# Kernel tuning notes

Measured on AMD Instinct MI355X. Metric: run time of the kernel, lower is better.

## Reference

```python
import jax, jax.numpy as jnp
import numpy as np

E = 256   # embed_dim
H = 8     # num_heads
D = E // H  # head_dim = 32
L = 1024  # seq len (Q_len == K_len == V_len)


def setup_inputs() -> dict:
    key = jax.random.key(0)
    ks = jax.random.split(key, 10)
    f = lambda k, s: jax.random.normal(k, s, dtype=jnp.float32)
    return {
        "V": f(ks[0], (L, E)),
        "K": f(ks[1], (L, E)),
        "Q": f(ks[2], (L, E)),
        # genomic-style coordinates, strictly positive
        "position": jax.random.uniform(ks[3], (L,), dtype=jnp.float32) * 1e5,
        "Wq": f(ks[4], (E, E)) * 0.02,
        "Wk": f(ks[5], (E, E)) * 0.02,
        "Wv": f(ks[6], (E, E)) * 0.02,
        "Wr": f(ks[7], (E, 1)) * 0.02,   # K_relative_linear weight [out=E, in=1]
        "Wo": f(ks[8], (E, E)) * 0.02,
        "bo": jnp.zeros((E,), jnp.float32),
    }


def reference(V, K, Q, position, Wq, Wk, Wv, Wr, Wo, bo):
    Lq = Q.shape[0]
    # projections (nn.Linear: x @ W.T), split into heads -> (L, H, D)
    q = (Q @ Wq.T).reshape(Lq, H, D)
    k = (K @ Wk.T).reshape(Lq, H, D)
    v = (V @ Wv.T).reshape(Lq, H, D)

    # relative position scalar per (q, k) pair: log(|p_q - p_k| + 1)
    rel = jnp.log(jnp.abs(position[:, None] - position[None, :]) + 1.0)  # (L, L)

    # K_relative_linear maps scalar rel -> (H, D); the einsum
    # 'nqhd,nhqjd->nhqj' then factorizes exactly as:
    #   sum_d Q[q,h,d] * rel[q,j] * Wr[h,d] = (Q . Wr)[h,q] * rel[q,j]
    # so we avoid materializing the (H, L, L, D) tensor while computing
    # mathematically identical results.
    Wr_h = Wr[:, 0].reshape(H, D)                    # (H, D)
    coeff = jnp.einsum('qhd,hd->hq', q, Wr_h)        # (H, L)

    energy = jnp.einsum('qhd,khd->hqk', q, k)        # (H, L, L)
    energy = energy + coeff[:, :, None] * rel[None, :, :]

    attn = jax.nn.softmax(energy / np.float32(E) ** 0.5, axis=2)
    out = jnp.einsum('hqk,khd->qhd', attn, v).reshape(Lq, E)
    out = out @ Wo.T + bo
    return out
```

## Files before the change

kernel.cpp:

```cpp
#include <hip/hip_runtime.h>
#include <math.h>

#define EDIM 256
#define LDIM 1024
#define HDIM 8
#define DDIM 32

typedef __attribute__((ext_vector_type(8))) short short8;
typedef __attribute__((ext_vector_type(4))) short shortx4;
typedef __attribute__((ext_vector_type(4))) float f32x4;

__device__ inline unsigned short bf16h(float x) {
    unsigned u = __float_as_uint(x);
    return (unsigned short)((u + 0x7fff + ((u >> 16) & 1)) >> 16);
}
__device__ inline float bf16tof(unsigned short h) {
    return __uint_as_float(((unsigned)h) << 16);
}
__device__ inline float exp2fast(float x) {
    float r; asm volatile("v_exp_f32 %0, %1" : "=v"(r) : "v"(x)); return r;
}
__device__ inline float log2fast(float x) {
    float r; asm volatile("v_log_f32 %0, %1" : "=v"(r) : "v"(x)); return r;
}

#define SC2 0.09016843880556021f

__global__ __launch_bounds__(256) void proj_kernel(
    const float* __restrict__ Q, const float* __restrict__ Km, const float* __restrict__ V,
    const float* __restrict__ Wq, const float* __restrict__ Wk, const float* __restrict__ Wv,
    const float* __restrict__ Wr, const float* __restrict__ Wo,
    short* __restrict__ qThi, short* __restrict__ qTlo,
    short* __restrict__ kThi, short* __restrict__ kTlo,
    short* __restrict__ vThi, short* __restrict__ vTlo,
    float* __restrict__ coeff, short* __restrict__ Wohi, short* __restrict__ Wolo)
{
    const int z = blockIdx.z;
    const int tid = threadIdx.x;

    if (z == 3) {
        const int idx = ((blockIdx.y * 32 + blockIdx.x) << 8) + tid;
        const float w = Wo[idx];
        const unsigned short hh = bf16h(w);
        Wohi[idx] = (short)hh;
        Wolo[idx] = (short)bf16h(w - bf16tof(hh));
        return;
    }

    const float* __restrict__ X = (z == 0) ? Q : (z == 1) ? Km : V;
    const float* __restrict__ W = (z == 0) ? Wq : (z == 1) ? Wk : Wv;
    short* __restrict__ dhi     = (z == 0) ? qThi : (z == 1) ? kThi : vThi;
    short* __restrict__ dlo     = (z == 0) ? qTlo : (z == 1) ? kTlo : vTlo;

    const int n0 = blockIdx.x * 32;
    const int o0 = blockIdx.y * 32;
    const int wave = tid >> 6, lane = tid & 63;
    const int n = lane & 15, quad = lane >> 4;
    const int rh = wave & 1, oh = wave >> 1;

    const int s    = tid >> 7;
    const int r    = (tid >> 2) & 31;
    const int qd   = tid & 3;
    const int half = r >> 4;
    const int fl8  = ((r & 15) | (qd << 4)) * 8;

    __shared__ short Xhi[2][2][512], Xlo[2][2][512];
    __shared__ short Whi[2][2][512], Wlo[2][2][512];
    __shared__ float cpart[2][2][16];

    const float* xp = X + (n0 + r) * EDIM + s * 32 + qd * 8;
    const float* wp = W + (o0 + r) * EDIM + s * 32 + qd * 8;

    float4 xa0 = *(const float4*)xp, xa1 = *(const float4*)(xp + 4);
    float4 wa0 = *(const float4*)wp, wa1 = *(const float4*)(wp + 4);

    f32x4 acc = {0.f, 0.f, 0.f, 0.f};

    for (int kb = 0; kb < EDIM; kb += 64) {
        __syncthreads();
        {
            float xv[8] = {xa0.x,xa0.y,xa0.z,xa0.w, xa1.x,xa1.y,xa1.z,xa1.w};
            float wv[8] = {wa0.x,wa0.y,wa0.z,wa0.w, wa1.x,wa1.y,wa1.z,wa1.w};
            short8 xh, xl, wh, wl;
            #pragma unroll
            for (int j = 0; j < 8; ++j) {
                unsigned short xhh = bf16h(xv[j]);
                unsigned short whh = bf16h(wv[j]);
                xh[j] = (short)xhh; xl[j] = (short)bf16h(xv[j] - bf16tof(xhh));
                wh[j] = (short)whh; wl[j] = (short)bf16h(wv[j] - bf16tof(whh));
            }
            *(short8*)&Xhi[s][half][fl8] = xh;
            *(short8*)&Xlo[s][half][fl8] = xl;
            *(short8*)&Whi[s][half][fl8] = wh;
            *(short8*)&Wlo[s][half][fl8] = wl;
        }
        float4 xn0, xn1, wn0, wn1;
        if (kb + 64 < EDIM) {
            xn0 = *(const float4*)(xp + kb + 64); xn1 = *(const float4*)(xp + kb + 68);
            wn0 = *(const float4*)(wp + kb + 64); wn1 = *(const float4*)(wp + kb + 68);
        }
        __syncthreads();
        #pragma unroll
        for (int ss = 0; ss < 2; ++ss) {
            short8 ah = *(const short8*)&Xhi[ss][rh][lane*8];
            short8 al = *(const short8*)&Xlo[ss][rh][lane*8];
            short8 bh = *(const short8*)&Whi[ss][oh][lane*8];
            short8 bl = *(const short8*)&Wlo[ss][oh][lane*8];
            acc = __builtin_amdgcn_mfma_f32_16x16x32_bf16(al, bh, acc, 0, 0, 0);
            acc = __builtin_amdgcn_mfma_f32_16x16x32_bf16(ah, bl, acc, 0, 0, 0);
            acc = __builtin_amdgcn_mfma_f32_16x16x32_bf16(ah, bh, acc, 0, 0, 0);
        }
        xa0 = xn0; xa1 = xn1; wa0 = wn0; wa1 = wn1;
    }

    const int h  = o0 >> 5;
    const int og = oh * 16 + n;
    #pragma unroll
    for (int i = 0; i < 4; ++i) {
        const int row = rh * 16 + 4 * quad + i;
        const unsigned short hh = bf16h(acc[i]);
        dhi[(h * LDIM + n0 + row) * DDIM + og] = (short)hh;
        dlo[(h * LDIM + n0 + row) * DDIM + og] = (short)bf16h(acc[i] - bf16tof(hh));
    }

    if (z == 0) {
        const float wr = Wr[o0 + og];
        #pragma unroll
        for (int i = 0; i < 4; ++i) {
            float c = acc[i] * wr;
            c += __shfl_xor(c, 1, 64);
            c += __shfl_xor(c, 2, 64);
            c += __shfl_xor(c, 4, 64);
            c += __shfl_xor(c, 8, 64);
            if (n == 0) cpart[rh][oh][4*quad + i] = c;
        }
        __syncthreads();
        if (tid < 32)
            coeff[h * LDIM + n0 + tid] = cpart[tid >> 4][0][tid & 15]
                                       + cpart[tid >> 4][1][tid & 15];
    }
}

__global__ __launch_bounds__(256, 4) void attn_kernel(
    const short* __restrict__ qThi, const short* __restrict__ qTlo,
    const short* __restrict__ kThi, const short* __restrict__ kTlo,
    const short* __restrict__ vThi, const short* __restrict__ vTlo,
    const float* __restrict__ coeff, const float* __restrict__ pos,
    float* __restrict__ Op, float* __restrict__ Mp, float* __restrict__ Lp, int nkt)
{
    const int h   = blockIdx.y;
    const int q0  = blockIdx.x * 64;
    const int p   = blockIdx.z;
    const int kt0 = p * nkt * 64;
    const int tid  = threadIdx.x;
    const int wave = tid >> 6;
    const int lane = tid & 63;
    const int n    = lane & 15;
    const int quad = lane >> 4;
    const int qs0  = wave * 16;

    __shared__ __align__(16) short khi[4*64*8];
    __shared__ __align__(16) short klo[4*64*8];
    __shared__ __align__(16) short vs_hi[32][72];
    __shared__ __align__(16) short vs_lo[32][72];
    __shared__ __align__(16) short pa_hi[64][72];
    __shared__ __align__(16) short pa_lo[64][72];
    __shared__ float pk[64];

    const short8 qhi = *(const short8*)(qThi + (h*LDIM + q0 + qs0 + n) * DDIM + quad*8);
    const short8 qlo = *(const short8*)(qTlo + (h*LDIM + q0 + qs0 + n) * DDIM + quad*8);

    float pq[4], cq[4];
    #pragma unroll
    for (int i = 0; i < 4; ++i) {
        const int r = q0 + qs0 + 4*quad + i;
        pq[i] = pos[r];
        cq[i] = coeff[h*LDIM + r] * 0.0625f;
    }

    float m[4], l[4];
    #pragma unroll
    for (int i = 0; i < 4; ++i) { m[i] = -INFINITY; l[i] = 0.f; }

    f32x4 of0 = {0.f,0.f,0.f,0.f}, of1 = {0.f,0.f,0.f,0.f};

    const int cS = tid >> 2;
    const int dq = tid & 3;
    const int lane2 = (cS & 15) | (dq << 4);
    const int gS = cS >> 4;

    short8 khi_c, klo_c, vhi_c, vlo_c; float pkc = 0.f;
    {
        const int off = (h*LDIM + kt0 + cS) * DDIM + dq*8;
        khi_c = *(const short8*)(kThi + off);
        klo_c = *(const short8*)(kTlo + off);
        vhi_c = *(const short8*)(vThi + off);
        vlo_c = *(const short8*)(vTlo + off);
        if (tid < 64) pkc = pos[kt0 + tid];
    }

    for (int t = 0; t < nkt; ++t) {
        __syncthreads();

        *((short8*)&khi[(gS*64 + lane2)*8]) = khi_c;
        *((short8*)&klo[(gS*64 + lane2)*8]) = klo_c;
        #pragma unroll
        for (int j = 0; j < 8; ++j) {
            vs_hi[dq*8 + j][cS] = vhi_c[j];
            vs_lo[dq*8 + j][cS] = vlo_c[j];
        }
        if (tid < 64) pk[tid] = pkc;

        short8 khi_n, klo_n, vhi_n, vlo_n; float pkn = 0.f;
        if (t + 1 < nkt) {
            const int off = (h*LDIM + kt0 + (t+1)*64 + cS) * DDIM + dq*8;
            khi_n = *(const short8*)(kThi + off);
            klo_n = *(const short8*)(kTlo + off);
            vhi_n = *(const short8*)(vThi + off);
            vlo_n = *(const short8*)(vTlo + off);
            if (tid < 64) pkn = pos[kt0 + (t+1)*64 + tid];
        }
        __syncthreads();

        f32x4 Sf[4];
        #pragma unroll
        for (int t4 = 0; t4 < 4; ++t4) {
            short8 bhi = *((const short8*)&khi[(t4*64 + lane)*8]);
            short8 blo = *((const short8*)&klo[(t4*64 + lane)*8]);
            f32x4 acc = {0.f, 0.f, 0.f, 0.f};
            acc = __builtin_amdgcn_mfma_f32_16x16x32_bf16(qlo, bhi, acc, 0, 0, 0);
            acc = __builtin_amdgcn_mfma_f32_16x16x32_bf16(qhi, blo, acc, 0, 0, 0);
            acc = __builtin_amdgcn_mfma_f32_16x16x32_bf16(qhi, bhi, acc, 0, 0, 0);
            Sf[t4] = acc;
        }

        float ev[4][4];
        float rmax[4] = {-INFINITY, -INFINITY, -INFINITY, -INFINITY};
        #pragma unroll
        for (int t4 = 0; t4 < 4; ++t4) {
            const float pkt = pk[16*t4 + n];
            #pragma unroll
            for (int i = 0; i < 4; ++i) {
                float s = fmaf(Sf[t4][i], SC2, cq[i] * log2fast(fabsf(pq[i] - pkt) + 1.f));
                ev[t4][i] = s;
                rmax[i] = fmaxf(rmax[i], s);
            }
        }
        #pragma unroll
        for (int off = 1; off < 16; off <<= 1)
            #pragma unroll
            for (int i = 0; i < 4; ++i)
                rmax[i] = fmaxf(rmax[i], __shfl_xor(rmax[i], off, 64));

        float al[4], rsum[4];
        #pragma unroll
        for (int i = 0; i < 4; ++i) {
            const float mn = fmaxf(m[i], rmax[i]);
            al[i] = exp2fast(m[i] - mn);
            m[i] = mn;
            rsum[i] = 0.f;
        }
        #pragma unroll
        for (int t4 = 0; t4 < 4; ++t4)
            #pragma unroll
            for (int i = 0; i < 4; ++i) {
                float e = exp2fast(ev[t4][i] - m[i]);
                rsum[i] += e;
                unsigned u = __float_as_uint(e);
                pa_hi[qs0 + 4*quad + i][16*t4 + n] = (short)(u >> 16);
                float r = e - __uint_as_float(u & 0xffff0000u);
                pa_lo[qs0 + 4*quad + i][16*t4 + n] = (short)bf16h(r);
            }
        #pragma unroll
        for (int off = 1; off < 16; off <<= 1)
            #pragma unroll
            for (int i = 0; i < 4; ++i)
                rsum[i] += __shfl_xor(rsum[i], off, 64);
        #pragma unroll
        for (int i = 0; i < 4; ++i) l[i] = l[i]*al[i] + rsum[i];

        #pragma unroll
        for (int i = 0; i < 4; ++i) { of0[i] *= al[i]; of1[i] *= al[i]; }

        #pragma unroll
        for (int ch = 0; ch < 2; ++ch) {
            short8 phi = *(const short8*)&pa_hi[qs0 + n][ch*32 + quad*8];
            short8 plo = *(const short8*)&pa_lo[qs0 + n][ch*32 + quad*8];
            #pragma unroll
            for (int dt = 0; dt < 2; ++dt) {
                short8 vh8 = *(const short8*)&vs_hi[dt*16 + n][ch*32 + quad*8];
                short8 vl8 = *(const short8*)&vs_lo[dt*16 + n][ch*32 + quad*8];
                f32x4& of = dt ? of1 : of0;
                of = __builtin_amdgcn_mfma_f32_16x16x32_bf16(plo, vh8, of, 0, 0, 0);
                of = __builtin_amdgcn_mfma_f32_16x16x32_bf16(phi, vl8, of, 0, 0, 0);
                of = __builtin_amdgcn_mfma_f32_16x16x32_bf16(phi, vh8, of, 0, 0, 0);
            }
        }

        khi_c = khi_n; klo_c = klo_n; vhi_c = vhi_n; vlo_c = vlo_n; pkc = pkn;
    }

    const int ph = p * HDIM + h;
    {
        const size_t base = ((size_t)ph * LDIM + q0 + qs0) * DDIM;
        #pragma unroll
        for (int i = 0; i < 4; ++i) {
            Op[base + (size_t)(4*quad + i)*DDIM + n]      = of0[i];
            Op[base + (size_t)(4*quad + i)*DDIM + 16 + n] = of1[i];
        }
    }
    if (n == 0) {
        #pragma unroll
        for (int i = 0; i < 4; ++i) {
            const int r = q0 + qs0 + 4*quad + i;
            Mp[ph*LDIM + r] = m[i];
            Lp[ph*LDIM + r] = l[i];
        }
    }
}

__global__ __launch_bounds__(256) void combine_kernel(
    const float* __restrict__ Op, const float* __restrict__ Mp, const float* __restrict__ Lp,
    int P, short* __restrict__ Ahi, short* __restrict__ Alo)
{
    const int idx = blockIdx.x * 256 + threadIdx.x;
    const int n  = idx >> 6;
    const int e4 = (idx & 63) * 4;
    const int h  = e4 >> 5;
    const int d  = e4 & 31;

    float mv[8], lv[8];
    float mx = -INFINITY;
    #pragma unroll
    for (int p = 0; p < 8; ++p) if (p < P) {
        mv[p] = Mp[(p*HDIM + h)*LDIM + n];
        lv[p] = Lp[(p*HDIM + h)*LDIM + n];
        mx = fmaxf(mx, mv[p]);
    }
    float s = 0.f;
    #pragma unroll
    for (int p = 0; p < 8; ++p) if (p < P) {
        float a = exp2fast(mv[p] - mx);
        mv[p] = a;
        s += a * lv[p];
    }
    const float inv = 1.f / s;

    float4 x; x.x = x.y = x.z = x.w = 0.f;
    #pragma unroll
    for (int p = 0; p < 8; ++p) if (p < P) {
        const float sp = mv[p] * inv;
        float4 xp = *(const float4*)(Op + ((size_t)(p*HDIM + h)*LDIM + n)*DDIM + d);
        x.x += sp*xp.x; x.y += sp*xp.y; x.z += sp*xp.z; x.w += sp*xp.w;
    }
    float a4[4] = {x.x, x.y, x.z, x.w};
    shortx4 ah4, al4;
    #pragma unroll
    for (int j = 0; j < 4; ++j) {
        const unsigned short hh = bf16h(a4[j]);
        ah4[j] = (short)hh;
        al4[j] = (short)bf16h(a4[j] - bf16tof(hh));
    }
    *(shortx4*)(Ahi + n*EDIM + e4) = ah4;
    *(shortx4*)(Alo + n*EDIM + e4) = al4;
}

__global__ __launch_bounds__(256) void outproj_kernel(
    const short* __restrict__ Ahi, const short* __restrict__ Alo,
    const short* __restrict__ Wohi, const short* __restrict__ Wolo,
    const float* __restrict__ bo, float* __restrict__ out)
{
    const int n0 = blockIdx.x * 32;
    const int o0 = blockIdx.y * 32;
    const int tid = threadIdx.x;
    const int wave = tid >> 6, lane = tid & 63;
    const int n = lane & 15, quad = lane >> 4;
    const int rh = wave & 1, oh = wave >> 1;

    const int s    = tid >> 7;
    const int r    = (tid >> 2) & 31;
    const int qd   = tid & 3;
    const int half = r >> 4;
    const int fl8  = ((r & 15) | (qd << 4)) * 8;

    __shared__ short Xhi[2][2][512], Xlo[2][2][512];
    __shared__ short Whi[2][2][512], Wlo[2][2][512];

    const short* xph = Ahi  + (n0 + r) * EDIM + s * 32 + qd * 8;
    const short* xpl = Alo  + (n0 + r) * EDIM + s * 32 + qd * 8;
    const short* wph = Wohi + (o0 + r) * EDIM + s * 32 + qd * 8;
    const short* wpl = Wolo + (o0 + r) * EDIM + s * 32 + qd * 8;

    short8 xh_c = *(const short8*)xph;
    short8 xl_c = *(const short8*)xpl;
    short8 wh_c = *(const short8*)wph;
    short8 wl_c = *(const short8*)wpl;

    f32x4 acc = {0.f, 0.f, 0.f, 0.f};

    for (int kb = 0; kb < EDIM; kb += 64) {
        __syncthreads();
        *(short8*)&Xhi[s][half][fl8] = xh_c;
        *(short8*)&Xlo[s][half][fl8] = xl_c;
        *(short8*)&Whi[s][half][fl8] = wh_c;
        *(short8*)&Wlo[s][half][fl8] = wl_c;
        short8 xh_n, xl_n, wh_n, wl_n;
        if (kb + 64 < EDIM) {
            xh_n = *(const short8*)(xph + kb + 64);
            xl_n = *(const short8*)(xpl + kb + 64);
            wh_n = *(const short8*)(wph + kb + 64);
            wl_n = *(const short8*)(wpl + kb + 64);
        }
        __syncthreads();
        #pragma unroll
        for (int ss = 0; ss < 2; ++ss) {
            short8 ah = *(const short8*)&Xhi[ss][rh][lane*8];
            short8 al = *(const short8*)&Xlo[ss][rh][lane*8];
            short8 bh = *(const short8*)&Whi[ss][oh][lane*8];
            short8 bl = *(const short8*)&Wlo[ss][oh][lane*8];
            acc = __builtin_amdgcn_mfma_f32_16x16x32_bf16(al, bh, acc, 0, 0, 0);
            acc = __builtin_amdgcn_mfma_f32_16x16x32_bf16(ah, bl, acc, 0, 0, 0);
            acc = __builtin_amdgcn_mfma_f32_16x16x32_bf16(ah, bh, acc, 0, 0, 0);
        }
        xh_c = xh_n; xl_c = xl_n; wh_c = wh_n; wl_c = wl_n;
    }

    const int og = o0 + oh*16 + n;
    const float b = bo[og];
    #pragma unroll
    for (int i = 0; i < 4; ++i) {
        const int row = n0 + rh*16 + 4*quad + i;
        out[row * EDIM + og] = acc[i] + b;
    }
}

extern "C" void kernel_launch(void* const* d_in, const int* in_sizes, int n_in,
                              void* d_out, int out_size, void* d_ws, size_t ws_size,
                              hipStream_t stream) {
    const float* V   = (const float*)d_in[0];
    const float* K   = (const float*)d_in[1];
    const float* Q   = (const float*)d_in[2];
    const float* pos = (const float*)d_in[3];
    const float* Wq  = (const float*)d_in[4];
    const float* Wk  = (const float*)d_in[5];
    const float* Wv  = (const float*)d_in[6];
    const float* Wr  = (const float*)d_in[7];
    const float* Wo  = (const float*)d_in[8];
    const float* bo  = (const float*)d_in[9];
    float* out = (float*)d_out;
    char* base = (char*)d_ws;

    auto need = [](int P) -> size_t { return 3440640 + (size_t)P * 1114112; };
    int P = 2;
    if (ws_size >= need(8)) P = 8;
    else if (ws_size >= need(4)) P = 4;

    short* qThi  = (short*)(base);
    short* qTlo  = (short*)(base + 524288);
    short* kThi  = (short*)(base + 1048576);
    short* kTlo  = (short*)(base + 1572864);
    short* vThi  = (short*)(base + 2097152);
    short* vTlo  = (short*)(base + 2621440);
    float* coeff = (float*)(base + 3145728);
    short* Wohi  = (short*)(base + 3178496);
    short* Wolo  = (short*)(base + 3309568);
    float* Op    = (float*)(base + 3440640);
    float* Mp    = Op + (size_t)P * 262144;
    float* Lp    = Mp + (size_t)P * 8192;
    short* Ahi   = qThi;
    short* Alo   = qTlo;

    proj_kernel   <<<dim3(32, 8, 4), 256, 0, stream>>>(Q, K, V, Wq, Wk, Wv, Wr, Wo,
                                                       qThi, qTlo, kThi, kTlo, vThi, vTlo,
                                                       coeff, Wohi, Wolo);
    attn_kernel   <<<dim3(16, 8, P), 256, 0, stream>>>(qThi, qTlo, kThi, kTlo, vThi, vTlo,
                                                       coeff, pos, Op, Mp, Lp, 16 / P);
    combine_kernel<<<dim3(256),      256, 0, stream>>>(Op, Mp, Lp, P, Ahi, Alo);
    outproj_kernel<<<dim3(32, 8),    256, 0, stream>>>(Ahi, Alo, Wohi, Wolo, bo, out);
}
```

Before: 104.6 us.

## Fuse split-K combine into attention with intra-block per-wave key splits

The attention kernel now gives each block 16 queries and splits the 1024 keys across its 4 waves, each wave running its own online softmax over 256 keys. The per-wave partial outputs, maxima and sums are merged in shared memory, and the result is written directly as bf16 hi/lo into A. This removes the separate combine kernel, one launch, and the global round-trip of partial outputs. In exchange K and the key positions are read straight from global memory with no shared staging, V is transposed per wave, and launch bounds drop to 2 blocks per CU.

```diff
diff --git a/kernel.cpp b/kernel.cpp
--- a/kernel.cpp
+++ b/kernel.cpp
@@ -7,6 +7,7 @@
 #define DDIM 32
 
 typedef __attribute__((ext_vector_type(8))) short short8;
+typedef __attribute__((ext_vector_type(2))) short short2v;
 typedef __attribute__((ext_vector_type(4))) short shortx4;
 typedef __attribute__((ext_vector_type(4))) float f32x4;
 
@@ -141,39 +142,35 @@
     }
 }
 
-__global__ __launch_bounds__(256, 4) void attn_kernel(
+__global__ __launch_bounds__(256, 2) void attn_kernel(
     const short* __restrict__ qThi, const short* __restrict__ qTlo,
     const short* __restrict__ kThi, const short* __restrict__ kTlo,
     const short* __restrict__ vThi, const short* __restrict__ vTlo,
     const float* __restrict__ coeff, const float* __restrict__ pos,
-    float* __restrict__ Op, float* __restrict__ Mp, float* __restrict__ Lp, int nkt)
+    short* __restrict__ Ahi, short* __restrict__ Alo)
 {
-    const int h   = blockIdx.y;
-    const int q0  = blockIdx.x * 64;
-    const int p   = blockIdx.z;
-    const int kt0 = p * nkt * 64;
+    const int h    = blockIdx.y;
+    const int q0   = blockIdx.x * 16;
     const int tid  = threadIdx.x;
     const int wave = tid >> 6;
     const int lane = tid & 63;
     const int n    = lane & 15;
     const int quad = lane >> 4;
-    const int qs0  = wave * 16;
-
-    __shared__ __align__(16) short khi[4*64*8];
-    __shared__ __align__(16) short klo[4*64*8];
-    __shared__ __align__(16) short vs_hi[32][72];
-    __shared__ __align__(16) short vs_lo[32][72];
-    __shared__ __align__(16) short pa_hi[64][72];
-    __shared__ __align__(16) short pa_lo[64][72];
-    __shared__ float pk[64];
-
-    const short8 qhi = *(const short8*)(qThi + (h*LDIM + q0 + qs0 + n) * DDIM + quad*8);
-    const short8 qlo = *(const short8*)(qTlo + (h*LDIM + q0 + qs0 + n) * DDIM + quad*8);
+
+    __shared__ __align__(16) short vs_hi[4][32][72];
+    __shared__ __align__(16) short vs_lo[4][32][72];
+    __shared__ __align__(16) short pa_hi[4][16][72];
+    __shared__ __align__(16) short pa_lo[4][16][72];
+    __shared__ float mw[4][16], lw[4][16];
+    __shared__ float Ow[4][16][36];
+
+    const short8 qhi = *(const short8*)(qThi + (h*LDIM + q0 + n) * DDIM + quad*8);
+    const short8 qlo = *(const short8*)(qTlo + (h*LDIM + q0 + n) * DDIM + quad*8);
 
     float pq[4], cq[4];
     #pragma unroll
     for (int i = 0; i < 4; ++i) {
-        const int r = q0 + qs0 + 4*quad + i;
+        const int r = q0 + 4*quad + i;
         pq[i] = pos[r];
         cq[i] = coeff[h*LDIM + r] * 0.0625f;
     }
@@ -181,56 +178,42 @@
     float m[4], l[4];
     #pragma unroll
     for (int i = 0; i < 4; ++i) { m[i] = -INFINITY; l[i] = 0.f; }
-
     f32x4 of0 = {0.f,0.f,0.f,0.f}, of1 = {0.f,0.f,0.f,0.f};
 
-    const int cS = tid >> 2;
-    const int dq = tid & 3;
-    const int lane2 = (cS & 15) | (dq << 4);
-    const int gS = cS >> 4;
-
-    short8 khi_c, klo_c, vhi_c, vlo_c; float pkc = 0.f;
-    {
-        const int off = (h*LDIM + kt0 + cS) * DDIM + dq*8;
-        khi_c = *(const short8*)(kThi + off);
-        klo_c = *(const short8*)(kTlo + off);
-        vhi_c = *(const short8*)(vThi + off);
-        vlo_c = *(const short8*)(vTlo + off);
-        if (tid < 64) pkc = pos[kt0 + tid];
-    }
-
-    for (int t = 0; t < nkt; ++t) {
-        __syncthreads();
-
-        *((short8*)&khi[(gS*64 + lane2)*8]) = khi_c;
-        *((short8*)&klo[(gS*64 + lane2)*8]) = klo_c;
-        #pragma unroll
-        for (int j = 0; j < 8; ++j) {
-            vs_hi[dq*8 + j][cS] = vhi_c[j];
-            vs_lo[dq*8 + j][cS] = vlo_c[j];
-        }
-        if (tid < 64) pk[tid] = pkc;
-
-        short8 khi_n, klo_n, vhi_n, vlo_n; float pkn = 0.f;
-        if (t + 1 < nkt) {
-            const int off = (h*LDIM + kt0 + (t+1)*64 + cS) * DDIM + dq*8;
-            khi_n = *(const short8*)(kThi + off);
-            klo_n = *(const short8*)(kTlo + off);
-            vhi_n = *(const short8*)(vThi + off);
-            vlo_n = *(const short8*)(vTlo + off);
-            if (tid < 64) pkn = pos[kt0 + (t+1)*64 + tid];
-        }
-        __syncthreads();
+    const int ktb = wave * 256;
+    #pragma unroll 1
+    for (int t = 0; t < 4; ++t) {
+        const int kt = ktb + t * 64;
+
+        {
+            const short* vh = vThi + (h*LDIM + kt + lane) * DDIM;
+            const short* vl = vTlo + (h*LDIM + kt + lane) * DDIM;
+            #pragma unroll
+            for (int hf = 0; hf < 2; ++hf) {
+                short8 a0 = *(const short8*)(vh + hf*16);
+                short8 a1 = *(const short8*)(vh + hf*16 + 8);
+                short8 b0 = *(const short8*)(vl + hf*16);
+                short8 b1 = *(const short8*)(vl + hf*16 + 8);
+                #pragma unroll
+                for (int j = 0; j < 8; ++j) {
+                    vs_hi[wave][hf*16 + j][lane]     = a0[j];
+                    vs_hi[wave][hf*16 + 8 + j][lane] = a1[j];
+                    vs_lo[wave][hf*16 + j][lane]     = b0[j];
+                    vs_lo[wave][hf*16 + 8 + j][lane] = b1[j];
+                }
+            }
+        }
 
         f32x4 Sf[4];
         #pragma unroll
         for (int t4 = 0; t4 < 4; ++t4) {
-            short8 bhi = *((const short8*)&khi[(t4*64 + lane)*8]);
-            short8 blo = *((const short8*)&klo[(t4*64 + lane)*8]);
+            const int off = (h*LDIM + kt + t4*16 + n) * DDIM + quad*8;
+            short8 bh = *(const short8*)(kThi + off);
+            short8 bl = *(const short8*)(kTlo + off);
             f32x4 acc = {0.f, 0.f, 0.f, 0.f};
-            acc = __builtin_amdgcn_mfma_f32_16x16x32_bf16(qlo, bhi, acc, 0, 0, 0);
-            acc = __builtin_amdgcn_mfma_f32_16x16x32_bf16(qhi, blo, acc, 0, 0, 0);
-            acc = __builtin_amdgcn_mfma_f32_16x16x32_bf16(qhi, bhi, acc, 0, 0, 0);
+            acc = __builtin_amdgcn_mfma_f32_16x16x32_bf16(qlo, bh, acc, 0, 0, 0);
+            acc = __builtin_amdgcn_mfma_f32_16x16x32_bf16(qhi, bl, acc, 0, 0, 0);
+            acc = __builtin_amdgcn_mfma_f32_16x16x32_bf16(qhi, bh, acc, 0, 0, 0);
             Sf[t4] = acc;
         }
 
@@ -238,7 +221,7 @@
         float rmax[4] = {-INFINITY, -INFINITY, -INFINITY, -INFINITY};
         #pragma unroll
         for (int t4 = 0; t4 < 4; ++t4) {
-            const float pkt = pk[16*t4 + n];
+            const float pkt = pos[kt + t4*16 + n];
             #pragma unroll
             for (int i = 0; i < 4; ++i) {
                 float s = fmaf(Sf[t4][i], SC2, cq[i] * log2fast(fabsf(pq[i] - pkt) + 1.f));
@@ -267,9 +250,9 @@
                 float e = exp2fast(ev[t4][i] - m[i]);
                 rsum[i] += e;
                 unsigned u = __float_as_uint(e);
-                pa_hi[qs0 + 4*quad + i][16*t4 + n] = (short)(u >> 16);
+                pa_hi[wave][4*quad + i][16*t4 + n] = (short)(u >> 16);
                 float r = e - __uint_as_float(u & 0xffff0000u);
-                pa_lo[qs0 + 4*quad + i][16*t4 + n] = (short)bf16h(r);
+                pa_lo[wave][4*quad + i][16*t4 + n] = (short)bf16h(r);
             }
         #pragma unroll
         for (int off = 1; off < 16; off <<= 1)
@@ -284,85 +267,59 @@
 
         #pragma unroll
         for (int ch = 0; ch < 2; ++ch) {
-            short8 phi = *(const short8*)&pa_hi[qs0 + n][ch*32 + quad*8];
-            short8 plo = *(const short8*)&pa_lo[qs0 + n][ch*32 + quad*8];
+            short8 phi = *(const short8*)&pa_hi[wave][n][ch*32 + quad*8];
+            short8 plo = *(const short8*)&pa_lo[wave][n][ch*32 + quad*8];
             #pragma unroll
             for (int dt = 0; dt < 2; ++dt) {
-                short8 vh8 = *(const short8*)&vs_hi[dt*16 + n][ch*32 + quad*8];
-                short8 vl8 = *(const short8*)&vs_lo[dt*16 + n][ch*32 + quad*8];
+                short8 vh8 = *(const short8*)&vs_hi[wave][dt*16 + n][ch*32 + quad*8];
+                short8 vl8 = *(const short8*)&vs_lo[wave][dt*16 + n][ch*32 + quad*8];
                 f32x4& of = dt ? of1 : of0;
                 of = __builtin_amdgcn_mfma_f32_16x16x32_bf16(plo, vh8, of, 0, 0, 0);
                 of = __builtin_amdgcn_mfma_f32_16x16x32_bf16(phi, vl8, of, 0, 0, 0);
                 of = __builtin_amdgcn_mfma_f32_16x16x32_bf16(phi, vh8, of, 0, 0, 0);
             }
         }
-
-        khi_c = khi_n; klo_c = klo_n; vhi_c = vhi_n; vlo_c = vlo_n; pkc = pkn;
-    }
-
-    const int ph = p * HDIM + h;
+    }
+
+    #pragma unroll
+    for (int i = 0; i < 4; ++i) {
+        Ow[wave][4*quad + i][n]      = of0[i];
+        Ow[wave][4*quad + i][16 + n] = of1[i];
+    }
+    if (n == 0) {
+        #pragma unroll
+        for (int i = 0; i < 4; ++i) {
+            mw[wave][4*quad + i] = m[i];
+            lw[wave][4*quad + i] = l[i];
+        }
+    }
+    __syncthreads();
+
     {
-        const size_t base = ((size_t)ph * LDIM + q0 + qs0) * DDIM;
-        #pragma unroll
-        for (int i = 0; i < 4; ++i) {
-            Op[base + (size_t)(4*quad + i)*DDIM + n]      = of0[i];
-            Op[base + (size_t)(4*quad + i)*DDIM + 16 + n] = of1[i];
-        }
-    }
-    if (n == 0) {
-        #pragma unroll
-        for (int i = 0; i < 4; ++i) {
-            const int r = q0 + qs0 + 4*quad + i;
-            Mp[ph*LDIM + r] = m[i];
-            Lp[ph*LDIM + r] = l[i];
-        }
-    }
-}
-
-__global__ __launch_bounds__(256) void combine_kernel(
-    const float* __restrict__ Op, const float* __restrict__ Mp, const float* __restrict__ Lp,
-    int P, short* __restrict__ Ahi, short* __restrict__ Alo)
-{
-    const int idx = blockIdx.x * 256 + threadIdx.x;
-    const int n  = idx >> 6;
-    const int e4 = (idx & 63) * 4;
-    const int h  = e4 >> 5;
-    const int d  = e4 & 31;
-
-    float mv[8], lv[8];
-    float mx = -INFINITY;
-    #pragma unroll
-    for (int p = 0; p < 8; ++p) if (p < P) {
-        mv[p] = Mp[(p*HDIM + h)*LDIM + n];
-        lv[p] = Lp[(p*HDIM + h)*LDIM + n];
-        mx = fmaxf(mx, mv[p]);
-    }
-    float s = 0.f;
-    #pragma unroll
-    for (int p = 0; p < 8; ++p) if (p < P) {
-        float a = exp2fast(mv[p] - mx);
-        mv[p] = a;
-        s += a * lv[p];
-    }
-    const float inv = 1.f / s;
-
-    float4 x; x.x = x.y = x.z = x.w = 0.f;
-    #pragma unroll
-    for (int p = 0; p < 8; ++p) if (p < P) {
-        const float sp = mv[p] * inv;
-        float4 xp = *(const float4*)(Op + ((size_t)(p*HDIM + h)*LDIM + n)*DDIM + d);
-        x.x += sp*xp.x; x.y += sp*xp.y; x.z += sp*xp.z; x.w += sp*xp.w;
-    }
-    float a4[4] = {x.x, x.y, x.z, x.w};
-    shortx4 ah4, al4;
-    #pragma unroll
-    for (int j = 0; j < 4; ++j) {
-        const unsigned short hh = bf16h(a4[j]);
-        ah4[j] = (short)hh;
-        al4[j] = (short)bf16h(a4[j] - bf16tof(hh));
-    }
-    *(shortx4*)(Ahi + n*EDIM + e4) = ah4;
-    *(shortx4*)(Alo + n*EDIM + e4) = al4;
+        const int q  = tid >> 4;
+        const int dp = (tid & 15) * 2;
+        float M = fmaxf(fmaxf(mw[0][q], mw[1][q]), fmaxf(mw[2][q], mw[3][q]));
+        float sc[4], s = 0.f;
+        #pragma unroll
+        for (int w = 0; w < 4; ++w) {
+            sc[w] = exp2fast(mw[w][q] - M);
+            s += sc[w] * lw[w][q];
+        }
+        const float inv = 1.f / s;
+        short2v h2, l2;
+        #pragma unroll
+        for (int e = 0; e < 2; ++e) {
+            float a = 0.f;
+            #pragma unroll
+            for (int w = 0; w < 4; ++w) a += sc[w] * Ow[w][q][dp + e];
+            a *= inv;
+            const unsigned short hh = bf16h(a);
+            h2[e] = (short)hh;
+            l2[e] = (short)bf16h(a - bf16tof(hh));
+        }
+        *(short2v*)(Ahi + (q0 + q)*EDIM + h*DDIM + dp) = h2;
+        *(short2v*)(Alo + (q0 + q)*EDIM + h*DDIM + dp) = l2;
+    }
 }
 
 __global__ __launch_bounds__(256) void outproj_kernel(
@@ -450,11 +407,6 @@
     float* out = (float*)d_out;
     char* base = (char*)d_ws;
 
-    auto need = [](int P) -> size_t { return 3440640 + (size_t)P * 1114112; };
-    int P = 2;
-    if (ws_size >= need(8)) P = 8;
-    else if (ws_size >= need(4)) P = 4;
-
     short* qThi  = (short*)(base);
     short* qTlo  = (short*)(base + 524288);
     short* kThi  = (short*)(base + 1048576);
@@ -464,17 +416,13 @@
     float* coeff = (float*)(base + 3145728);
     short* Wohi  = (short*)(base + 3178496);
     short* Wolo  = (short*)(base + 3309568);
-    float* Op    = (float*)(base + 3440640);
-    float* Mp    = Op + (size_t)P * 262144;
-    float* Lp    = Mp + (size_t)P * 8192;
-    short* Ahi   = qThi;
-    short* Alo   = qTlo;
+    short* Ahi   = (short*)(base + 3440640);
+    short* Alo   = (short*)(base + 3964928);
 
     proj_kernel   <<<dim3(32, 8, 4), 256, 0, stream>>>(Q, K, V, Wq, Wk, Wv, Wr, Wo,
                                                        qThi, qTlo, kThi, kTlo, vThi, vTlo,
                                                        coeff, Wohi, Wolo);
-    attn_kernel   <<<dim3(16, 8, P), 256, 0, stream>>>(qThi, qTlo, kThi, kTlo, vThi, vTlo,
-                                                       coeff, pos, Op, Mp, Lp, 16 / P);
-    combine_kernel<<<dim3(256),      256, 0, stream>>>(Op, Mp, Lp, P, Ahi, Alo);
+    attn_kernel   <<<dim3(64, 8),    256, 0, stream>>>(qThi, qTlo, kThi, kTlo, vThi, vTlo,
+                                                       coeff, pos, Ahi, Alo);
     outproj_kernel<<<dim3(32, 8),    256, 0, stream>>>(Ahi, Alo, Wohi, Wolo, bo, out);
 }
```

After: 101.0 us (median of 2 runs). -3.4%, faster.
